# Kernel optimization log

Measured on AMD Instinct MI355X. Metric: run time of the kernel, lower is better.

The kernel has to match this reference:

```python
import jax, jax.numpy as jnp
import numpy as np

N_NODES = 50000
N_EDGES = 800000
D_FEAT = 64


def setup_inputs() -> dict:
    key = jax.random.key(0)
    k1, k2, k3, k4 = jax.random.split(key, 4)
    row_idx = jnp.sort(jax.random.randint(k1, (N_EDGES,), 0, N_NODES, dtype=jnp.int32))
    col_idx = jax.random.randint(k2, (N_EDGES,), 0, N_NODES, dtype=jnp.int32)
    vals = jax.random.uniform(k3, (N_EDGES,), dtype=jnp.float32)
    embeds = jax.random.normal(k4, (N_NODES, D_FEAT), dtype=jnp.float32)
    return {"row_idx": row_idx, "col_idx": col_idx, "vals": vals, "embeds": embeds}


def reference(row_idx, col_idx, vals, embeds):
    # SpMM: out[r] = sum_{e: row[e]==r} vals[e] * embeds[col[e]]
    gathered = vals[:, None] * embeds[col_idx]          # [E, D]
    out = jax.ops.segment_sum(gathered, row_idx, num_segments=N_NODES)  # [N, D]
    return out
```

## Files before the change

### kernel.cpp

```cpp
#include <hip/hip_runtime.h>


constexpr int N_NODES = 50000;
constexpr int N_EDGES = 800000;
constexpr int D_FEAT  = 64;

using uvec4 = __attribute__((ext_vector_type(4))) unsigned int;
using fvec4 = __attribute__((ext_vector_type(4))) float;

constexpr size_t WS_ROWPTR_OFF = 0;
constexpr size_t WS_TBL_OFF    = 1u << 20;
constexpr size_t WS_SCALE_OFF  = 5u << 20;

constexpr int ROWPTR_BLOCKS = (N_EDGES + 255) / 256;
constexpr int QUANT_BLOCKS  = (N_NODES + 3) / 4;

__global__ __launch_bounds__(256) void prep_kernel(
    const int*   __restrict__ row_idx,
    const float* __restrict__ embeds,
    int*         __restrict__ row_ptr,
    signed char* __restrict__ tbl,
    float*       __restrict__ scales)
{
    if (blockIdx.x < ROWPTR_BLOCKS) {
        const int e = blockIdx.x * 256 + threadIdx.x;
        if (e >= N_EDGES) return;
        const int r     = row_idx[e];
        const int rprev = (e == 0) ? -1 : row_idx[e - 1];
        for (int q = rprev + 1; q <= r; ++q) row_ptr[q] = e;
        if (e == N_EDGES - 1) {
            for (int q = r + 1; q <= N_NODES; ++q) row_ptr[q] = N_EDGES;
        }
    } else {
        const int r = (blockIdx.x - ROWPTR_BLOCKS) * 4 + (threadIdx.x >> 6);
        if (r >= N_NODES) return;
        const int lane = threadIdx.x & 63;
        const float x = embeds[r * D_FEAT + lane];
        float m = fabsf(x);
#pragma unroll
        for (int mask = 1; mask < 64; mask <<= 1)
            m = fmaxf(m, __shfl_xor(m, mask));
        const float qs = (m > 0.f) ? 127.f / m : 0.f;
        const int   q  = (int)rintf(x * qs);
        tbl[r * D_FEAT + lane] = (signed char)q;
        if (lane == 0) scales[r] = (m > 0.f) ? m / 127.f : 0.f;
    }
}

__global__ __launch_bounds__(256) void gcn_spmm_kernel(
    const int*         __restrict__ row_ptr,
    const int*         __restrict__ col_idx,
    const float*       __restrict__ vals,
    const signed char* __restrict__ tbl,
    const float*       __restrict__ scales,
    float*             __restrict__ out)
{
    const int row = blockIdx.x * 4 + (threadIdx.x >> 6);
    if (row >= N_NODES) return;

    const int lane = threadIdx.x & 63;
    const int g    = lane >> 2;
    const int h    = lane & 3;

    const int es = __builtin_amdgcn_readfirstlane(row_ptr[row]);
    const int ee = __builtin_amdgcn_readfirstlane(row_ptr[row + 1]);

    const uvec4* __restrict__ tbl16 = (const uvec4*)tbl;

    float acc[16];
#pragma unroll
    for (int i = 0; i < 16; ++i) acc[i] = 0.f;

    for (int base = es; base < ee; base += 32) {
        const int e0 = base + g;
        const int e1 = base + 16 + g;
        const int i0 = (e0 < ee) ? e0 : ee - 1;
        const int i1 = (e1 < ee) ? e1 : ee - 1;
        const int c0 = col_idx[i0];
        const int c1 = col_idx[i1];
        const float v0 = (e0 < ee) ? vals[i0] : 0.f;
        const float v1 = (e1 < ee) ? vals[i1] : 0.f;
        const uvec4 q0 = tbl16[c0 * 4 + h];
        const uvec4 q1 = tbl16[c1 * 4 + h];
        const float w0 = v0 * scales[c0];
        const float w1 = v1 * scales[c1];
#pragma unroll
        for (int wd = 0; wd < 4; ++wd) {
#pragma unroll
            for (int b = 0; b < 4; ++b) {
                acc[wd * 4 + b] +=
                    w0 * (float)(signed char)((q0[wd] >> (8 * b)) & 0xff);
                acc[wd * 4 + b] +=
                    w1 * (float)(signed char)((q1[wd] >> (8 * b)) & 0xff);
            }
        }
    }

    float a8[8];
    {
        const int b = g & 1;
#pragma unroll
        for (int j = 0; j < 8; ++j) {
            const float send = b ? acc[2 * j] : acc[2 * j + 1];
            const float keep = b ? acc[2 * j + 1] : acc[2 * j];
            a8[j] = keep + __shfl_xor(send, 4);
        }
    }
    float a4[4];
    {
        const int b = (g >> 1) & 1;
#pragma unroll
        for (int j = 0; j < 4; ++j) {
            const float send = b ? a8[2 * j] : a8[2 * j + 1];
            const float keep = b ? a8[2 * j + 1] : a8[2 * j];
            a4[j] = keep + __shfl_xor(send, 8);
        }
    }
    float a2[2];
    {
        const int b = (g >> 2) & 1;
#pragma unroll
        for (int j = 0; j < 2; ++j) {
            const float send = b ? a4[2 * j] : a4[2 * j + 1];
            const float keep = b ? a4[2 * j + 1] : a4[2 * j];
            a2[j] = keep + __shfl_xor(send, 16);
        }
    }
    float a1;
    {
        const int b = (g >> 3) & 1;
        const float send = b ? a2[0] : a2[1];
        const float keep = b ? a2[1] : a2[0];
        a1 = keep + __shfl_xor(send, 32);
    }

    __builtin_nontemporal_store(a1, out + row * D_FEAT + h * 16 + g);
}

extern "C" void kernel_launch(void* const* d_in, const int* in_sizes, int n_in,
                              void* d_out, int out_size, void* d_ws, size_t ws_size,
                              hipStream_t stream) {
    const int*   row_idx = (const int*)  d_in[0];
    const int*   col_idx = (const int*)  d_in[1];
    const float* vals    = (const float*)d_in[2];
    const float* embeds  = (const float*)d_in[3];
    float*       out     = (float*)      d_out;

    char* ws = (char*)d_ws;
    int*         row_ptr = (int*)        (ws + WS_ROWPTR_OFF);
    signed char* tbl     = (signed char*)(ws + WS_TBL_OFF);
    float*       scales  = (float*)      (ws + WS_SCALE_OFF);

    prep_kernel<<<ROWPTR_BLOCKS + QUANT_BLOCKS, 256, 0, stream>>>(
        row_idx, embeds, row_ptr, tbl, scales);

    gcn_spmm_kernel<<<(N_NODES + 3) / 4, 256, 0, stream>>>(
        row_ptr, col_idx, vals, tbl, scales, out);
}
```

Measured before the change: 99.09 us.

## Replace int8-with-scale embedding table by bf16 table and packed FMA accumulation

Converts embeddings to a bf16 table instead of per-row int8 quantization with scales, so the prep pass drops the 64-lane max-reduction and the SpMM drops the per-column scale load. The SpMM remaps lanes to 8 edges by 8 column chunks, processes up to four 8-edge groups per iteration with early-exit guards, and accumulates with v_pk_fma_f32 on bf16-expanded pairs. In exchange, the gathered table is twice as large (128 B per row), so gather traffic doubles. Accuracy improves relative to int8.

```diff
diff --git a/kernel.cpp b/kernel.cpp
--- a/kernel.cpp
+++ b/kernel.cpp
@@ -7,20 +7,27 @@
 
 using uvec4 = __attribute__((ext_vector_type(4))) unsigned int;
 using fvec4 = __attribute__((ext_vector_type(4))) float;
+using f32x2 = __attribute__((ext_vector_type(2))) float;
 
 constexpr size_t WS_ROWPTR_OFF = 0;
 constexpr size_t WS_TBL_OFF    = 1u << 20;
-constexpr size_t WS_SCALE_OFF  = 5u << 20;
 
 constexpr int ROWPTR_BLOCKS = (N_EDGES + 255) / 256;
-constexpr int QUANT_BLOCKS  = (N_NODES + 3) / 4;
+constexpr int CONV_THREADS  = N_NODES * D_FEAT / 8;
+constexpr int CONV_BLOCKS   = (CONV_THREADS + 255) / 256;
+
+__device__ inline unsigned pack_bf16x2(float a, float b) {
+    unsigned ua = __float_as_uint(a), ub = __float_as_uint(b);
+    ua = (ua + 0x7fffu + ((ua >> 16) & 1u)) >> 16;
+    ub = (ub + 0x7fffu + ((ub >> 16) & 1u)) & 0xffff0000u;
+    return ua | ub;
+}
 
 __global__ __launch_bounds__(256) void prep_kernel(
-    const int*   __restrict__ row_idx,
-    const float* __restrict__ embeds,
-    int*         __restrict__ row_ptr,
-    signed char* __restrict__ tbl,
-    float*       __restrict__ scales)
+    const int*      __restrict__ row_idx,
+    const float*    __restrict__ embeds,
+    int*            __restrict__ row_ptr,
+    unsigned short* __restrict__ tbl)
 {
     if (blockIdx.x < ROWPTR_BLOCKS) {
         const int e = blockIdx.x * 256 + threadIdx.x;
@@ -32,93 +39,82 @@
             for (int q = r + 1; q <= N_NODES; ++q) row_ptr[q] = N_EDGES;
         }
     } else {
-        const int r = (blockIdx.x - ROWPTR_BLOCKS) * 4 + (threadIdx.x >> 6);
-        if (r >= N_NODES) return;
-        const int lane = threadIdx.x & 63;
-        const float x = embeds[r * D_FEAT + lane];
-        float m = fabsf(x);
-#pragma unroll
-        for (int mask = 1; mask < 64; mask <<= 1)
-            m = fmaxf(m, __shfl_xor(m, mask));
-        const float qs = (m > 0.f) ? 127.f / m : 0.f;
-        const int   q  = (int)rintf(x * qs);
-        tbl[r * D_FEAT + lane] = (signed char)q;
-        if (lane == 0) scales[r] = (m > 0.f) ? m / 127.f : 0.f;
+        const int t = (blockIdx.x - ROWPTR_BLOCKS) * 256 + threadIdx.x;
+        if (t >= CONV_THREADS) return;
+        const fvec4* __restrict__ src = (const fvec4*)embeds;
+        const fvec4 x0 = src[t * 2];
+        const fvec4 x1 = src[t * 2 + 1];
+        uvec4 p;
+        p[0] = pack_bf16x2(x0[0], x0[1]);
+        p[1] = pack_bf16x2(x0[2], x0[3]);
+        p[2] = pack_bf16x2(x1[0], x1[1]);
+        p[3] = pack_bf16x2(x1[2], x1[3]);
+        ((uvec4*)tbl)[t] = p;
     }
 }
 
 __global__ __launch_bounds__(256) void gcn_spmm_kernel(
-    const int*         __restrict__ row_ptr,
-    const int*         __restrict__ col_idx,
-    const float*       __restrict__ vals,
-    const signed char* __restrict__ tbl,
-    const float*       __restrict__ scales,
-    float*             __restrict__ out)
+    const int*            __restrict__ row_ptr,
+    const int*            __restrict__ col_idx,
+    const float*          __restrict__ vals,
+    const unsigned short* __restrict__ tbl,
+    float*                __restrict__ out)
 {
     const int row = blockIdx.x * 4 + (threadIdx.x >> 6);
     if (row >= N_NODES) return;
 
     const int lane = threadIdx.x & 63;
-    const int g    = lane >> 2;
-    const int h    = lane & 3;
+    const int g    = lane >> 3;
+    const int h    = lane & 7;
 
     const int es = __builtin_amdgcn_readfirstlane(row_ptr[row]);
     const int ee = __builtin_amdgcn_readfirstlane(row_ptr[row + 1]);
 
     const uvec4* __restrict__ tbl16 = (const uvec4*)tbl;
 
-    float acc[16];
+    f32x2 acc[4];
 #pragma unroll
-    for (int i = 0; i < 16; ++i) acc[i] = 0.f;
+    for (int i = 0; i < 4; ++i) { acc[i][0] = 0.f; acc[i][1] = 0.f; }
 
     for (int base = es; base < ee; base += 32) {
-        const int e0 = base + g;
-        const int e1 = base + 16 + g;
-        const int i0 = (e0 < ee) ? e0 : ee - 1;
-        const int i1 = (e1 < ee) ? e1 : ee - 1;
-        const int c0 = col_idx[i0];
-        const int c1 = col_idx[i1];
-        const float v0 = (e0 < ee) ? vals[i0] : 0.f;
-        const float v1 = (e1 < ee) ? vals[i1] : 0.f;
-        const uvec4 q0 = tbl16[c0 * 4 + h];
-        const uvec4 q1 = tbl16[c1 * 4 + h];
-        const float w0 = v0 * scales[c0];
-        const float w1 = v1 * scales[c1];
 #pragma unroll
-        for (int wd = 0; wd < 4; ++wd) {
+        for (int k = 0; k < 4; ++k) {
+            if (base + k * 8 < ee) {
+                const int e = base + k * 8 + g;
+                const int i = (e < ee) ? e : ee - 1;
+                const int c = col_idx[i];
+                const float v = (e < ee) ? vals[i] : 0.f;
+                const uvec4 q = tbl16[c * 8 + h];
+                f32x2 w; w[0] = v; w[1] = v;
 #pragma unroll
-            for (int b = 0; b < 4; ++b) {
-                acc[wd * 4 + b] +=
-                    w0 * (float)(signed char)((q0[wd] >> (8 * b)) & 0xff);
-                acc[wd * 4 + b] +=
-                    w1 * (float)(signed char)((q1[wd] >> (8 * b)) & 0xff);
+                for (int d = 0; d < 4; ++d) {
+                    f32x2 f;
+                    f[0] = __uint_as_float(q[d] << 16);
+                    f[1] = __uint_as_float(q[d] & 0xffff0000u);
+                    asm("v_pk_fma_f32 %0, %1, %2, %0"
+                        : "+v"(acc[d]) : "v"(w), "v"(f));
+                }
             }
         }
     }
 
-    float a8[8];
+    float a[8];
+#pragma unroll
+    for (int d = 0; d < 4; ++d) { a[2 * d] = acc[d][0]; a[2 * d + 1] = acc[d][1]; }
+
+    float a4[4];
     {
         const int b = g & 1;
 #pragma unroll
-        for (int j = 0; j < 8; ++j) {
-            const float send = b ? acc[2 * j] : acc[2 * j + 1];
-            const float keep = b ? acc[2 * j + 1] : acc[2 * j];
-            a8[j] = keep + __shfl_xor(send, 4);
-        }
-    }
-    float a4[4];
-    {
-        const int b = (g >> 1) & 1;
-#pragma unroll
         for (int j = 0; j < 4; ++j) {
-            const float send = b ? a8[2 * j] : a8[2 * j + 1];
-            const float keep = b ? a8[2 * j + 1] : a8[2 * j];
+            const float send = b ? a[2 * j] : a[2 * j + 1];
+            const float keep = b ? a[2 * j + 1] : a[2 * j];
             a4[j] = keep + __shfl_xor(send, 8);
         }
     }
     float a2[2];
     {
-        const int b = (g >> 2) & 1;
+        const int b = (g >> 1) & 1;
 #pragma unroll
         for (int j = 0; j < 2; ++j) {
             const float send = b ? a4[2 * j] : a4[2 * j + 1];
@@ -128,13 +124,13 @@
     }
     float a1;
     {
-        const int b = (g >> 3) & 1;
+        const int b = (g >> 2) & 1;
         const float send = b ? a2[0] : a2[1];
         const float keep = b ? a2[1] : a2[0];
         a1 = keep + __shfl_xor(send, 32);
     }
 
-    __builtin_nontemporal_store(a1, out + row * D_FEAT + h * 16 + g);
+    __builtin_nontemporal_store(a1, out + row * D_FEAT + h * 8 + g);
 }
 
 extern "C" void kernel_launch(void* const* d_in, const int* in_sizes, int n_in,
@@ -147,13 +143,12 @@
     float*       out     = (float*)      d_out;
 
     char* ws = (char*)d_ws;
-    int*         row_ptr = (int*)        (ws + WS_ROWPTR_OFF);
-    signed char* tbl     = (signed char*)(ws + WS_TBL_OFF);
-    float*       scales  = (float*)      (ws + WS_SCALE_OFF);
+    int*            row_ptr = (int*)           (ws + WS_ROWPTR_OFF);
+    unsigned short* tbl     = (unsigned short*)(ws + WS_TBL_OFF);
 
-    prep_kernel<<<ROWPTR_BLOCKS + QUANT_BLOCKS, 256, 0, stream>>>(
-        row_idx, embeds, row_ptr, tbl, scales);
+    prep_kernel<<<ROWPTR_BLOCKS + CONV_BLOCKS, 256, 0, stream>>>(
+        row_idx, embeds, row_ptr, tbl);
 
     gcn_spmm_kernel<<<(N_NODES + 3) / 4, 256, 0, stream>>>(
-        row_ptr, col_idx, vals, tbl, scales, out);
+        row_ptr, col_idx, vals, tbl, out);
 }
```

After: 96.91 us. 1.02x faster.
